# Optimization experiments

Measured on AMD Instinct MI355X. Metric: run time of the kernel, lower is better.

Reference implementation:

```python
import jax, jax.numpy as jnp
import numpy as np
import math

B, W, N = 48, 100, 1000
EMB, H, QKV, LOCAL = 128, 8, 16, 100
L = LOCAL + 1  # depot + local_size neighbors


def pos_enc(length):
    # sinusoidal positional encoding, emb_dim even so no pad needed
    nts = EMB // 2
    inv = jnp.exp(jnp.arange(nts, dtype=jnp.float32) * (-math.log(10000.0) / max(nts - 1, 1)))
    pos = jnp.arange(length, dtype=jnp.float32)
    st = pos[:, None] * inv[None, :]
    return jnp.concatenate([jnp.sin(st), jnp.cos(st)], axis=1)  # [length, EMB]


def setup_inputs() -> dict:
    key = jax.random.key(0)
    ks = jax.random.split(key, 11)
    return {
        "theta": jax.random.uniform(ks[0], (B, W, N), dtype=jnp.float32),
        "dist": jax.random.uniform(ks[1], (B, W, N), dtype=jnp.float32),
        "xy": jax.random.uniform(ks[2], (B, W, N, 2), dtype=jnp.float32),
        "norm_demand": jax.random.uniform(ks[3], (B, W, N), dtype=jnp.float32),
        "ninf_mask": jnp.zeros((B, W, N), jnp.float32),
        "init_w": jax.random.normal(ks[4], (3, EMB), dtype=jnp.float32) * 0.1,
        "init_b": jnp.zeros((EMB,), jnp.float32),
        "cur_token": jax.random.uniform(ks[5], (EMB,), minval=-1.0, maxval=1.0, dtype=jnp.float32),
        "Wq": jax.random.normal(ks[6], (EMB, H * QKV), dtype=jnp.float32) * 0.05,
        "Wk": jax.random.normal(ks[7], (EMB, H * QKV), dtype=jnp.float32) * 0.05,
        "Wv": jax.random.normal(ks[8], (EMB, H * QKV), dtype=jnp.float32) * 0.05,
        "Wc_w": jax.random.normal(ks[9], (H * QKV, EMB), dtype=jnp.float32) * 0.05,
        "Wc_b": jnp.zeros((EMB,), jnp.float32),
    }


def reference(theta, dist, xy, norm_demand, ninf_mask, init_w, init_b, cur_token, Wq, Wk, Wv, Wc_w, Wc_b):
    # depot always masked: dist -= mask => depot distance -> +inf
    mask = ninf_mask.at[:, :, 0].set(-jnp.inf)
    dist_eff = dist - mask  # [B,W,N]

    # k smallest distances among non-depot nodes (topk largest=False)
    neg_vals, idx0 = jax.lax.top_k(-dist_eff[:, :, 1:], LOCAL)
    dvals = -neg_vals
    dvals = jnp.where(jnp.isinf(dvals), 0.0, dvals)
    norm_on = (jnp.max(dvals, axis=-1) != 0.0)[..., None]          # [B,W,1]
    norm_fac = jnp.max(dvals, axis=-1, keepdims=True) + 1e-6       # [B,W,1]

    depot = jnp.zeros((B, W, 1), idx0.dtype)
    idx = jnp.concatenate([depot, idx0 + 1], axis=-1)              # [B,W,L]

    g = lambda a: jnp.take_along_axis(a, idx, axis=-1)
    sd = g(dist_eff)
    sdem = g(norm_demand)
    sm = g(ninf_mask)
    sx = g(xy[..., 0])
    sy = g(xy[..., 1])

    # zero out inf entries (the masked depot slot)
    infm = jnp.isinf(sd)
    sdem = jnp.where(infm, 0.0, sdem)
    sx = jnp.where(infm, 0.0, sx)
    sy = jnp.where(infm, 0.0, sy)

    # per-(b,w) coordinate normalization by max local distance
    sx = jnp.where(norm_on, sx / norm_fac, sx)
    sy = jnp.where(norm_on, sy / norm_fac, sy)

    # euclidean + demand => 3 input features
    sorted_input = jnp.stack([sx, sy, sdem], axis=-1)              # [B,W,L,3]
    init_k = sorted_input @ init_w + init_b + pos_enc(L)[None, None]  # [B,W,L,EMB]

    # cur_token is identical for every (b,w) -> shared query per head
    q = (cur_token @ Wq).reshape(H, QKV)
    k = (init_k @ Wk).reshape(B, W, L, H, QKV)
    v = (init_k @ Wv).reshape(B, W, L, H, QKV)

    score = jnp.einsum('hd,bwlhd->bwhl', q, k) / float(np.sqrt(QKV)) + sm[:, :, None, :]
    attn = jax.nn.softmax(score, axis=-1)
    out = jnp.einsum('bwhl,bwlhd->bwhd', attn, v).reshape(B, W, H * QKV)

    mh = out @ Wc_w + Wc_b                                         # [B,W,EMB]
    score2 = jnp.einsum('bwe,bwle->bwl', mh, init_k) / float(np.sqrt(EMB))

    bi = jnp.arange(B)[:, None, None]
    wi = jnp.arange(W)[None, :, None]
    return jnp.zeros((B, W, N), score2.dtype).at[bi, wi, idx].set(score2)
```

## Files before the change

kernel.cpp:

```cpp
#include <hip/hip_runtime.h>
#include <math.h>

#define Bb   48
#define Ww   100
#define Nn   1000
#define EMB  128
#define Hh   8
#define LL   101
#define LOCALK 100
#define TPB  128
#define PPB  2

typedef _Float16 half2v __attribute__((ext_vector_type(2)));
typedef _Float16 half8v __attribute__((ext_vector_type(8)));

#define WS_A    0
#define WS_PE   1024
#define WS_AC   13952
#define WS_WVI  13984
#define WS_PEA  14496
#define WS_PEH  15304
#define WS_PVH  21768
#define WS_WCT  28424

#define AR_SIZE 7584

#define WSYNC() do { __builtin_amdgcn_wave_barrier(); asm volatile("" ::: "memory"); } while (0)

__device__ __forceinline__ unsigned f2key(float x) {
    unsigned u = __float_as_uint(x);
    return (u & 0x80000000u) ? ~u : (u | 0x80000000u);
}
__device__ __forceinline__ float key2f(unsigned k) {
    unsigned u = (k & 0x80000000u) ? (k & 0x7fffffffu) : ~k;
    return __uint_as_float(u);
}
__device__ __forceinline__ void dot8(float& c0, float& c1, float& c2, float& c3,
                                     half8v p, half8v a) {
    c0 = __builtin_amdgcn_fdot2(__builtin_shufflevector(p, p, 0, 1),
                                __builtin_shufflevector(a, a, 0, 1), c0, false);
    c1 = __builtin_amdgcn_fdot2(__builtin_shufflevector(p, p, 2, 3),
                                __builtin_shufflevector(a, a, 2, 3), c1, false);
    c2 = __builtin_amdgcn_fdot2(__builtin_shufflevector(p, p, 4, 5),
                                __builtin_shufflevector(a, a, 4, 5), c2, false);
    c3 = __builtin_amdgcn_fdot2(__builtin_shufflevector(p, p, 6, 7),
                                __builtin_shufflevector(a, a, 6, 7), c3, false);
}

__global__ void setup1(const float* __restrict__ cur, const float* __restrict__ Wq,
                       const float* __restrict__ Wk, const float* __restrict__ iw,
                       const float* __restrict__ ib, const float* __restrict__ Wv,
                       float* __restrict__ ws) {
    const int t = threadIdx.x, b = blockIdx.x;
    if (b == 0) {
        __shared__ float qs[EMB];
        __shared__ float as_[Hh * EMB];
        if (t < EMB) {
            float acc = 0.f;
            for (int e = 0; e < EMB; ++e) acc += cur[e] * Wq[e * EMB + t];
            qs[t] = acc;
        }
        __syncthreads();
        for (int i = t; i < Hh * EMB; i += 256) {
            int h = i >> 7, e = i & 127;
            float acc = 0.f;
            for (int d = 0; d < 16; ++d) acc += Wk[e * EMB + h * 16 + d] * qs[h * 16 + d];
            acc *= 0.25f;
            as_[i] = acc; ws[WS_A + i] = acc;
        }
        __syncthreads();
        if (t < 32) {
            int i = t >> 3, h = t & 7;
            const float* src = (i == 0) ? iw : (i == 1) ? iw + EMB : (i == 2) ? iw + 2 * EMB : ib;
            float acc = 0.f;
            for (int e = 0; e < EMB; ++e) acc += src[e] * as_[h * EMB + e];
            ws[WS_AC + t] = acc;
        }
    } else {
        int base = (b - 1) * 256 + t;
        const float kneg = -0.14619587891040738f;
        if (base < LL * EMB) {
            int l = base >> 7, c = base & 127, ic = c & 63;
            float inv = expf((float)ic * kneg);
            float v = (float)l * inv;
            float r = (c < 64) ? sinf(v) : cosf(v);
            ws[WS_PE + base] = r;
            ((_Float16*)(ws + WS_PEH))[base] = (_Float16)r;
        } else if (base < LL * EMB + 512) {
            int j = base - LL * EMB;
            int iv = j >> 7, hd = j & 127;
            const float* src = (iv == 0) ? iw : (iv == 1) ? iw + EMB : (iv == 2) ? iw + 2 * EMB : ib;
            float acc = 0.f;
            for (int e = 0; e < EMB; ++e) acc += src[e] * Wv[e * EMB + hd];
            ws[WS_WVI + j] = acc;
        }
    }
}

__global__ void setup2a(const float* __restrict__ Wv, float* __restrict__ ws) {
    int idx = blockIdx.x * 256 + threadIdx.x;
    if (idx < 128 * 104) {
        int hd = idx / 104, l = idx - hd * 104;
        float acc = 0.f;
        if (l < LL) {
            const float* pr = ws + WS_PE + l * EMB;
            for (int e = 0; e < EMB; ++e) acc += pr[e] * Wv[e * EMB + hd];
        }
        ((_Float16*)(ws + WS_PVH))[idx] = (_Float16)acc;
    } else if (idx < 128 * 104 + Hh * LL) {
        int j = idx - 128 * 104;
        int h = j / LL, l = j - h * LL;
        const float* pr = ws + WS_PE + l * EMB;
        const float* ar = ws + WS_A + h * EMB;
        float acc = 0.f;
        for (int e = 0; e < EMB; ++e) acc += pr[e] * ar[e];
        ws[WS_PEA + j] = acc;
    }
}

__global__ void setup2b(const float* __restrict__ Wcw, float* __restrict__ ws) {
    int idx = blockIdx.x * 256 + threadIdx.x;
    if (idx < 128 * 128) {
        int e = idx >> 7, hd = idx & 127;
        ((_Float16*)(ws + WS_WCT))[idx] = (_Float16)Wcw[hd * EMB + e];
    }
}

__global__ __launch_bounds__(TPB, 5) void main_kernel(
    const float* __restrict__ dist,
    const float* __restrict__ xy,
    const float* __restrict__ ndem,
    const float* __restrict__ ninf,
    const float* __restrict__ iw,
    const float* __restrict__ ib,
    const float* __restrict__ Wcb,
    const float* __restrict__ ws,
    float* __restrict__ out) {

    __shared__ __align__(16) char smem[PPB][AR_SIZE];
    const int tid  = threadIdx.x;
    const int w    = tid >> 6;
    const int lane = tid & 63;
    const int bw   = blockIdx.x * PPB + w;

    char* A = smem[w];
    int*                hist4 = (int*)A;
    _Float16*           attnh = (_Float16*)A;
    _Float16*           uhh   = (_Float16*)(A + 1792);
    float*              row   = (float*)A;
    unsigned long long* list  = (unsigned long long*)(A + 4288);
    int*                sel   = (int*)(A + 5088);
    unsigned char*      perm  = (unsigned char*)(A + 5492);
    float*              smk   = (float*)(A + 5592);
    float*              feat3 = (float*)(A + 5996);
    _Float16*           mhh   = (_Float16*)(A + 7216);
    float*              coef  = (float*)(A + 7472);
    float*              coefM = (float*)(A + 7568);

    const float* distRow = dist + (size_t)bw * Nn;
    const float* maskRow = ninf + (size_t)bw * Nn;
    const float* xyRow   = xy   + (size_t)bw * Nn * 2;
    const float* demRow  = ndem + (size_t)bw * Nn;

    float dvf[16], mkf[16];
    {
        float4 dv[4], mv[4];
        #pragma unroll
        for (int c = 0; c < 4; ++c) {
            int n0 = c * 256 + lane * 4;
            if (n0 < Nn) {
                dv[c] = *(const float4*)(distRow + n0);
                mv[c] = *(const float4*)(maskRow + n0);
            } else {
                dv[c] = make_float4(0.f, 0.f, 0.f, 0.f);
                mv[c] = make_float4(0.f, 0.f, 0.f, 0.f);
            }
        }
        #pragma unroll
        for (int k = 0; k < 5; ++k) {
            int idx = lane + 64 * k;
            if (idx < 260) ((int4*)hist4)[idx] = make_int4(0, 0, 0, 0);
        }
        #pragma unroll
        for (int c = 0; c < 4; ++c) {
            dvf[4*c+0] = dv[c].x; dvf[4*c+1] = dv[c].y; dvf[4*c+2] = dv[c].z; dvf[4*c+3] = dv[c].w;
            mkf[4*c+0] = mv[c].x; mkf[4*c+1] = mv[c].y; mkf[4*c+2] = mv[c].z; mkf[4*c+3] = mv[c].w;
        }
    }
    unsigned long long rk[16];
    #pragma unroll
    for (int r = 0; r < 16; ++r) {
        int n = (r >> 2) * 256 + lane * 4 + (r & 3);
        unsigned long long kv = ~0ull;
        if (n >= 1 && n < Nn) {
            float de = dvf[r] - mkf[r];
            kv = ((unsigned long long)f2key(de) << 32) | (unsigned)n;
        }
        rk[r] = kv;
    }
    WSYNC();

    unsigned long long prefix = 0;
    int shift = 56;
    int remRank = 99;
    const unsigned long long ltm = (1ull << lane) - 1ull;
    const int g0 = (lane >> 4) * 260;
    for (int round = 0; round < 8; ++round) {
        shift = 56 - 8 * round;
        #pragma unroll
        for (int r = 0; r < 16; ++r) {
            unsigned long long kv = rk[r];
            bool in = (kv != ~0ull) &&
                      (round == 0 || (kv >> (shift + 8)) == (prefix >> (shift + 8)));
            if (in) atomicAdd(&hist4[g0 + (int)((kv >> shift) & 0xffull)], 1);
        }
        WSYNC();
        int4 h0 = *(int4*)&hist4[0 * 260 + 4 * lane];
        int4 h1 = *(int4*)&hist4[1 * 260 + 4 * lane];
        int4 h2 = *(int4*)&hist4[2 * 260 + 4 * lane];
        int4 h3 = *(int4*)&hist4[3 * 260 + 4 * lane];
        int4 z = make_int4(0, 0, 0, 0);
        *(int4*)&hist4[0 * 260 + 4 * lane] = z;
        *(int4*)&hist4[1 * 260 + 4 * lane] = z;
        *(int4*)&hist4[2 * 260 + 4 * lane] = z;
        *(int4*)&hist4[3 * 260 + 4 * lane] = z;
        int cx = h0.x + h1.x + h2.x + h3.x;
        int cy = h0.y + h1.y + h2.y + h3.y;
        int cz = h0.z + h1.z + h2.z + h3.z;
        int cw = h0.w + h1.w + h2.w + h3.w;
        int s = cx + cy + cz + cw;
        int incl = s;
        #pragma unroll
        for (int o = 1; o < 64; o <<= 1) { int t = __shfl_up(incl, o, 64); if (lane >= o) incl += t; }
        int e0 = incl - s;
        int e1 = e0 + cx, e2 = e1 + cy, e3 = e2 + cz;
        int bc = -1, ec = 0, cc = 0;
        if (cx > 0 && remRank >= e0 && remRank < e1)      { bc = 4*lane+0; ec = e0; cc = cx; }
        if (cy > 0 && remRank >= e1 && remRank < e2)      { bc = 4*lane+1; ec = e1; cc = cy; }
        if (cz > 0 && remRank >= e2 && remRank < e3)      { bc = 4*lane+2; ec = e2; cc = cz; }
        if (cw > 0 && remRank >= e3 && remRank < e3 + cw) { bc = 4*lane+3; ec = e3; cc = cw; }
        unsigned long long fm = __ballot(bc >= 0);
        int srcl = __ffsll((unsigned long long)fm) - 1;
        bc = __shfl(bc, srcl, 64); ec = __shfl(ec, srcl, 64); cc = __shfl(cc, srcl, 64);
        prefix |= ((unsigned long long)(unsigned)bc) << shift;
        remRank -= ec;
        if (cc == 1) break;
    }
    unsigned long long pk = 0; bool pf = false;
    #pragma unroll
    for (int r = 0; r < 16; ++r)
        if ((rk[r] >> shift) == (prefix >> shift)) { pk = rk[r]; pf = true; }
    {
        unsigned long long fm = __ballot(pf);
        int srcl = __ffsll((unsigned long long)fm) - 1;
        pk = __shfl(pk, srcl, 64);
    }
    const unsigned long long pivot = pk;

    int cnt_run = 0;
    #pragma unroll
    for (int r = 0; r < 16; ++r) {
        bool p = rk[r] <= pivot;
        unsigned long long m = __ballot(p);
        if (p) list[cnt_run + (int)__popcll(m & ltm)] = rk[r];
        cnt_run += (int)__popcll(m);
    }
    WSYNC();

    {
        unsigned long long kv0 = list[lane];
        const bool has1 = lane < (LOCALK - 64);
        unsigned long long kv1 = has1 ? list[lane + 64] : ~0ull;
        int r0 = 0, r1 = 0;
        #pragma unroll 4
        for (int j = 0; j < LOCALK; ++j) {
            unsigned long long lv = list[j];
            r0 += (lv < kv0);
            r1 += (lv < kv1);
        }
        float v0 = key2f((unsigned)(kv0 >> 32));
        float dvm = isinf(v0) ? 0.f : v0;
        perm[lane] = (unsigned char)(r0 + 1);
        if (has1) {
            float v1 = key2f((unsigned)(kv1 >> 32));
            perm[lane + 64] = (unsigned char)(r1 + 1);
            dvm = fmaxf(dvm, isinf(v1) ? 0.f : v1);
        }
        #pragma unroll
        for (int o = 32; o > 0; o >>= 1) dvm = fmaxf(dvm, __shfl_xor(dvm, o, 64));
        const float nmax = dvm;
        const bool  norm_on = (nmax != 0.f);
        const float nfac = nmax + 1e-6f;
        WSYNC();

        int crun = 0;
        #pragma unroll
        for (int half = 0; half < 2; ++half) {
            float xs[8], ys[8], dd[8];
            #pragma unroll
            for (int cl = 0; cl < 2; ++cl) {
                int c = half * 2 + cl;
                int n0 = c * 256 + lane * 4;
                float4 a0, a1, d0;
                if (n0 < Nn) {
                    a0 = *(const float4*)(xyRow + 2 * n0);
                    a1 = *(const float4*)(xyRow + 2 * n0 + 4);
                    d0 = *(const float4*)(demRow + n0);
                } else {
                    a0 = a1 = d0 = make_float4(0.f, 0.f, 0.f, 0.f);
                }
                xs[4*cl+0] = a0.x; ys[4*cl+0] = a0.y;
                xs[4*cl+1] = a0.z; ys[4*cl+1] = a0.w;
                xs[4*cl+2] = a1.x; ys[4*cl+2] = a1.y;
                xs[4*cl+3] = a1.z; ys[4*cl+3] = a1.w;
                dd[4*cl+0] = d0.x; dd[4*cl+1] = d0.y; dd[4*cl+2] = d0.z; dd[4*cl+3] = d0.w;
            }
            #pragma unroll
            for (int q = 0; q < 8; ++q) {
                int r = half * 8 + q;
                unsigned long long kv = rk[r];
                bool p = kv <= pivot;
                unsigned long long m = __ballot(p);
                int pos = crun + (int)__popcll(m & ltm);
                crun += (int)__popcll(m);
                if (p) {
                    int rnk = perm[pos];
                    float val = key2f((unsigned)(kv >> 32));
                    bool infm = isinf(val);
                    float fx = infm ? 0.f : xs[q];
                    float fy = infm ? 0.f : ys[q];
                    float fd = infm ? 0.f : dd[q];
                    if (norm_on) { fx /= nfac; fy /= nfac; }
                    int n = (int)(kv & 0xffffffu);
                    feat3[rnk] = fx; feat3[101 + rnk] = fy; feat3[202 + rnk] = fd;
                    smk[rnk] = mkf[r];
                    sel[rnk] = n | (infm ? 0x40000000 : 0);
                }
            }
        }
        if (lane == 0) {
            feat3[0] = 0.f; feat3[101] = 0.f; feat3[202] = 0.f;
            smk[0] = mkf[0];
            sel[0] = 0x40000000;
        }
    }
    WSYNC();

    const int h = lane >> 3, ln8 = lane & 7;
    {
        const float A0 = ws[WS_AC + h], A1 = ws[WS_AC + 8 + h];
        const float A2 = ws[WS_AC + 16 + h], Cc = ws[WS_AC + 24 + h];
        const float* pea = ws + WS_PEA + h * LL;
        float ev[14];
        float mx = -INFINITY;
        #pragma unroll
        for (int k = 0; k < 14; ++k) {
            int l = ln8 + 8 * k;
            float sv = -INFINITY;
            if (l < LL)
                sv = feat3[l] * A0 + feat3[101 + l] * A1 + feat3[202 + l] * A2
                   + Cc + pea[l] + smk[l];
            ev[k] = sv;
            mx = fmaxf(mx, sv);
        }
        #pragma unroll
        for (int o = 1; o < 8; o <<= 1) mx = fmaxf(mx, __shfl_xor(mx, o, 64));
        float sm = 0.f;
        #pragma unroll
        for (int k = 0; k < 14; ++k) {
            int l = ln8 + 8 * k;
            float e = (l < LL) ? __expf(ev[k] - mx) : 0.f;
            ev[k] = e; sm += e;
        }
        #pragma unroll
        for (int o = 1; o < 8; o <<= 1) sm += __shfl_xor(sm, o, 64);
        const float ainv = 1.f / sm;
        #pragma unroll
        for (int k = 0; k < 14; ++k) {
            int l = ln8 + 8 * k;
            attnh[h * 112 + l] = (_Float16)(ev[k] * ainv);
        }
        float c0 = 0.f, c1 = 0.f, c2 = 0.f;
        #pragma unroll
        for (int k = 0; k < 13; ++k) {
            int l = ln8 + 8 * k;
            if (l < LL) {
                float at = ev[k] * ainv;
                c0 += at * feat3[l]; c1 += at * feat3[101 + l]; c2 += at * feat3[202 + l];
            }
        }
        #pragma unroll
        for (int o = 1; o < 8; o <<= 1) {
            c0 += __shfl_xor(c0, o, 64); c1 += __shfl_xor(c1, o, 64); c2 += __shfl_xor(c2, o, 64);
        }
        if (ln8 == 0) { coef[h * 3 + 0] = c0; coef[h * 3 + 1] = c1; coef[h * 3 + 2] = c2; }
    }
    WSYNC();

    #pragma unroll
    for (int t = 0; t < 2; ++t) {
        int hd = lane + 64 * t;
        int hh = hd >> 4;
        const half8v* pv = (const half8v*)((const _Float16*)(ws + WS_PVH) + hd * 104);
        const half8v* at = (const half8v*)(attnh + hh * 112);
        float d0 = 0.f, d1 = 0.f, d2 = 0.f, d3 = 0.f;
        #pragma unroll
        for (int j = 0; j < 13; ++j) dot8(d0, d1, d2, d3, pv[j], at[j]);
        float u = (d0 + d1) + (d2 + d3)
                + coef[hh * 3 + 0] * ws[WS_WVI + hd]
                + coef[hh * 3 + 1] * ws[WS_WVI + 128 + hd]
                + coef[hh * 3 + 2] * ws[WS_WVI + 256 + hd]
                + ws[WS_WVI + 384 + hd];
        uhh[hd] = (_Float16)u;
    }
    WSYNC();

    #pragma unroll
    for (int t = 0; t < 2; ++t) {
        int e = lane + 64 * t;
        const half8v* wr = (const half8v*)((const _Float16*)(ws + WS_WCT) + e * 128);
        const half8v* ur = (const half8v*)uhh;
        float d0 = 0.f, d1 = 0.f, d2 = 0.f, d3 = 0.f;
        #pragma unroll
        for (int j = 0; j < 16; ++j) dot8(d0, d1, d2, d3, wr[j], ur[j]);
        mhh[e] = (_Float16)(Wcb[e] + (d0 + d1) + (d2 + d3));
    }
    WSYNC();

    {
        int g = lane & 3;
        const float* src = (g == 0) ? iw : (g == 1) ? iw + EMB : (g == 2) ? iw + 2 * EMB : ib;
        float v = 0.f;
        #pragma unroll
        for (int j = 0; j < 8; ++j) {
            int e = (lane >> 2) + 16 * j;
            v += (float)mhh[e] * src[e];
        }
        v += __shfl_xor(v, 4, 64); v += __shfl_xor(v, 8, 64);
        v += __shfl_xor(v, 16, 64); v += __shfl_xor(v, 32, 64);
        if (lane < 4) coefM[lane] = v;
    }
    {
        float4 z = make_float4(0.f, 0.f, 0.f, 0.f);
        ((float4*)row)[lane] = z;
        ((float4*)row)[lane + 64] = z;
        ((float4*)row)[lane + 128] = z;
        if (lane < 58) ((float4*)row)[lane + 192] = z;
    }
    WSYNC();

    auto score2 = [&](int t) {
        float base = feat3[t] * coefM[0] + feat3[101 + t] * coefM[1]
                   + feat3[202 + t] * coefM[2] + coefM[3];
        const half8v* pr = (const half8v*)((const _Float16*)(ws + WS_PEH) + t * 128);
        const half8v* mr = (const half8v*)mhh;
        float d0 = 0.f, d1 = 0.f, d2 = 0.f, d3 = 0.f;
        #pragma unroll
        for (int j = 0; j < 16; ++j) dot8(d0, d1, d2, d3, pr[j], mr[j]);
        row[sel[t] & 0xffffff] = (base + (d0 + d1) + (d2 + d3)) * 0.08838834764831845f;
    };
    score2(lane);
    if (lane < LL - 64) score2(lane + 64);
    WSYNC();

    float* outRow = out + (size_t)bw * Nn;
    ((float4*)outRow)[lane]       = ((float4*)row)[lane];
    ((float4*)outRow)[lane + 64]  = ((float4*)row)[lane + 64];
    ((float4*)outRow)[lane + 128] = ((float4*)row)[lane + 128];
    if (lane < 58) ((float4*)outRow)[lane + 192] = ((float4*)row)[lane + 192];
}

extern "C" void kernel_launch(void* const* d_in, const int* in_sizes, int n_in,
                              void* d_out, int out_size, void* d_ws, size_t ws_size,
                              hipStream_t stream) {
    const float* dist  = (const float*)d_in[1];
    const float* xy    = (const float*)d_in[2];
    const float* ndem  = (const float*)d_in[3];
    const float* ninf  = (const float*)d_in[4];
    const float* initw = (const float*)d_in[5];
    const float* initb = (const float*)d_in[6];
    const float* cur   = (const float*)d_in[7];
    const float* Wq    = (const float*)d_in[8];
    const float* Wk    = (const float*)d_in[9];
    const float* Wv    = (const float*)d_in[10];
    const float* Wcw   = (const float*)d_in[11];
    const float* Wcb   = (const float*)d_in[12];
    float* out = (float*)d_out;
    float* ws  = (float*)d_ws;

    hipLaunchKernelGGL(setup1,  dim3(56), dim3(256), 0, stream, cur, Wq, Wk, initw, initb, Wv, ws);
    hipLaunchKernelGGL(setup2a, dim3(56), dim3(256), 0, stream, Wv, ws);
    hipLaunchKernelGGL(setup2b, dim3(64), dim3(256), 0, stream, Wcw, ws);
    hipLaunchKernelGGL(main_kernel, dim3(Bb * Ww / PPB), dim3(TPB), 0, stream,
                       dist, xy, ndem, ninf, initw, initb, Wcb, ws, out);
}
```

Before: 101.6 us.

## Switch attention/projection dot products from fp16 fdot2 to fp32 with transposed layouts

```diff
diff --git a/kernel.cpp b/kernel.cpp
--- a/kernel.cpp
+++ b/kernel.cpp
@@ -11,19 +11,24 @@
 #define TPB  128
 #define PPB  2
 
-typedef _Float16 half2v __attribute__((ext_vector_type(2)));
-typedef _Float16 half8v __attribute__((ext_vector_type(8)));
+typedef float f4v __attribute__((ext_vector_type(4)));
 
 #define WS_A    0
 #define WS_PE   1024
 #define WS_AC   13952
 #define WS_WVI  13984
 #define WS_PEA  14496
-#define WS_PEH  15304
-#define WS_PVH  21768
-#define WS_WCT  28424
-
-#define AR_SIZE 7584
+#define WS_PVT  15304
+#define WS_PET  28232
+
+#define AR_SIZE 7840
+#define AR_SEL  5088
+#define AR_PERM 5492
+#define AR_SMK  5592
+#define AR_F3   5996
+#define AR_MHF  7208
+#define AR_COEF 7720
+#define AR_CM   7816
 
 #define WSYNC() do { __builtin_amdgcn_wave_barrier(); asm volatile("" ::: "memory"); } while (0)
 
@@ -34,17 +39,6 @@
 __device__ __forceinline__ float key2f(unsigned k) {
     unsigned u = (k & 0x80000000u) ? (k & 0x7fffffffu) : ~k;
     return __uint_as_float(u);
-}
-__device__ __forceinline__ void dot8(float& c0, float& c1, float& c2, float& c3,
-                                     half8v p, half8v a) {
-    c0 = __builtin_amdgcn_fdot2(__builtin_shufflevector(p, p, 0, 1),
-                                __builtin_shufflevector(a, a, 0, 1), c0, false);
-    c1 = __builtin_amdgcn_fdot2(__builtin_shufflevector(p, p, 2, 3),
-                                __builtin_shufflevector(a, a, 2, 3), c1, false);
-    c2 = __builtin_amdgcn_fdot2(__builtin_shufflevector(p, p, 4, 5),
-                                __builtin_shufflevector(a, a, 4, 5), c2, false);
-    c3 = __builtin_amdgcn_fdot2(__builtin_shufflevector(p, p, 6, 7),
-                                __builtin_shufflevector(a, a, 6, 7), c3, false);
 }
 
 __global__ void setup1(const float* __restrict__ cur, const float* __restrict__ Wq,
@@ -83,9 +77,7 @@
             int l = base >> 7, c = base & 127, ic = c & 63;
             float inv = expf((float)ic * kneg);
             float v = (float)l * inv;
-            float r = (c < 64) ? sinf(v) : cosf(v);
-            ws[WS_PE + base] = r;
-            ((_Float16*)(ws + WS_PEH))[base] = (_Float16)r;
+            ws[WS_PE + base] = (c < 64) ? sinf(v) : cosf(v);
         } else if (base < LL * EMB + 512) {
             int j = base - LL * EMB;
             int iv = j >> 7, hd = j & 127;
@@ -97,18 +89,20 @@
     }
 }
 
-__global__ void setup2a(const float* __restrict__ Wv, float* __restrict__ ws) {
+__global__ void setup2(const float* __restrict__ Wv, float* __restrict__ ws) {
     int idx = blockIdx.x * 256 + threadIdx.x;
-    if (idx < 128 * 104) {
-        int hd = idx / 104, l = idx - hd * 104;
+    if (idx < LL * EMB) {
+        int l = idx >> 7, hd = idx & 127;
+        const float* pr = ws + WS_PE + l * EMB;
         float acc = 0.f;
-        if (l < LL) {
-            const float* pr = ws + WS_PE + l * EMB;
-            for (int e = 0; e < EMB; ++e) acc += pr[e] * Wv[e * EMB + hd];
-        }
-        ((_Float16*)(ws + WS_PVH))[idx] = (_Float16)acc;
-    } else if (idx < 128 * 104 + Hh * LL) {
-        int j = idx - 128 * 104;
+        for (int e = 0; e < EMB; ++e) acc += pr[e] * Wv[e * EMB + hd];
+        ws[WS_PVT + idx] = acc;
+    } else if (idx < LL * EMB + 128 * 128) {
+        int j = idx - LL * EMB;
+        int e = j >> 7, l = j & 127;
+        ws[WS_PET + j] = (l < LL) ? ws[WS_PE + l * EMB + e] : 0.f;
+    } else if (idx < LL * EMB + 128 * 128 + Hh * LL) {
+        int j = idx - (LL * EMB + 128 * 128);
         int h = j / LL, l = j - h * LL;
         const float* pr = ws + WS_PE + l * EMB;
         const float* ar = ws + WS_A + h * EMB;
@@ -118,44 +112,45 @@
     }
 }
 
-__global__ void setup2b(const float* __restrict__ Wcw, float* __restrict__ ws) {
-    int idx = blockIdx.x * 256 + threadIdx.x;
-    if (idx < 128 * 128) {
-        int e = idx >> 7, hd = idx & 127;
-        ((_Float16*)(ws + WS_WCT))[idx] = (_Float16)Wcw[hd * EMB + e];
-    }
-}
-
-__global__ __launch_bounds__(TPB, 5) void main_kernel(
+__global__ __launch_bounds__(TPB, 4) void main_kernel(
     const float* __restrict__ dist,
     const float* __restrict__ xy,
     const float* __restrict__ ndem,
     const float* __restrict__ ninf,
     const float* __restrict__ iw,
     const float* __restrict__ ib,
+    const float* __restrict__ Wcw,
     const float* __restrict__ Wcb,
     const float* __restrict__ ws,
     float* __restrict__ out) {
 
     __shared__ __align__(16) char smem[PPB][AR_SIZE];
+    __shared__ __align__(16) float sPEA[Hh * LL + 32];
+
     const int tid  = threadIdx.x;
     const int w    = tid >> 6;
     const int lane = tid & 63;
-    const int bw   = blockIdx.x * PPB + w;
+    const int bid  = blockIdx.x;
+    const int bw   = ((bid & 7) * 300 + (bid >> 3)) * PPB + w;
+
+    for (int i = tid; i < Hh * LL + 32; i += TPB)
+        sPEA[i] = (i < Hh * LL) ? ws[WS_PEA + i] : ws[WS_AC + (i - Hh * LL)];
+    __syncthreads();
+    const float* sAC = sPEA + Hh * LL;
 
     char* A = smem[w];
     int*                hist4 = (int*)A;
-    _Float16*           attnh = (_Float16*)A;
-    _Float16*           uhh   = (_Float16*)(A + 1792);
+    float*              attnf = (float*)A;
+    float*              uhf   = (float*)(A + 3232);
     float*              row   = (float*)A;
     unsigned long long* list  = (unsigned long long*)(A + 4288);
-    int*                sel   = (int*)(A + 5088);
-    unsigned char*      perm  = (unsigned char*)(A + 5492);
-    float*              smk   = (float*)(A + 5592);
-    float*              feat3 = (float*)(A + 5996);
-    _Float16*           mhh   = (_Float16*)(A + 7216);
-    float*              coef  = (float*)(A + 7472);
-    float*              coefM = (float*)(A + 7568);
+    int*                sel   = (int*)(A + AR_SEL);
+    unsigned char*      perm  = (unsigned char*)(A + AR_PERM);
+    float*              smk   = (float*)(A + AR_SMK);
+    float*              feat3 = (float*)(A + AR_F3);
+    float*              mhf   = (float*)(A + AR_MHF);
+    float*              coef  = (float*)(A + AR_COEF);
+    float*              coefM = (float*)(A + AR_CM);
 
     const float* distRow = dist + (size_t)bw * Nn;
     const float* maskRow = ninf + (size_t)bw * Nn;
@@ -267,6 +262,27 @@
     }
     WSYNC();
 
+    float xs[16], ys[16], dd[16];
+    {
+        #pragma unroll
+        for (int c = 0; c < 4; ++c) {
+            int n0 = c * 256 + lane * 4;
+            float4 a0, a1, d0;
+            if (n0 < Nn) {
+                a0 = *(const float4*)(xyRow + 2 * n0);
+                a1 = *(const float4*)(xyRow + 2 * n0 + 4);
+                d0 = *(const float4*)(demRow + n0);
+            } else {
+                a0 = a1 = d0 = make_float4(0.f, 0.f, 0.f, 0.f);
+            }
+            xs[4*c+0] = a0.x; ys[4*c+0] = a0.y;
+            xs[4*c+1] = a0.z; ys[4*c+1] = a0.w;
+            xs[4*c+2] = a1.x; ys[4*c+2] = a1.y;
+            xs[4*c+3] = a1.z; ys[4*c+3] = a1.w;
+            dd[4*c+0] = d0.x; dd[4*c+1] = d0.y; dd[4*c+2] = d0.z; dd[4*c+3] = d0.w;
+        }
+    }
+
     {
         unsigned long long kv0 = list[lane];
         const bool has1 = lane < (LOCALK - 64);
@@ -295,47 +311,24 @@
 
         int crun = 0;
         #pragma unroll
-        for (int half = 0; half < 2; ++half) {
-            float xs[8], ys[8], dd[8];
-            #pragma unroll
-            for (int cl = 0; cl < 2; ++cl) {
-                int c = half * 2 + cl;
-                int n0 = c * 256 + lane * 4;
-                float4 a0, a1, d0;
-                if (n0 < Nn) {
-                    a0 = *(const float4*)(xyRow + 2 * n0);
-                    a1 = *(const float4*)(xyRow + 2 * n0 + 4);
-                    d0 = *(const float4*)(demRow + n0);
-                } else {
-                    a0 = a1 = d0 = make_float4(0.f, 0.f, 0.f, 0.f);
-                }
-                xs[4*cl+0] = a0.x; ys[4*cl+0] = a0.y;
-                xs[4*cl+1] = a0.z; ys[4*cl+1] = a0.w;
-                xs[4*cl+2] = a1.x; ys[4*cl+2] = a1.y;
-                xs[4*cl+3] = a1.z; ys[4*cl+3] = a1.w;
-                dd[4*cl+0] = d0.x; dd[4*cl+1] = d0.y; dd[4*cl+2] = d0.z; dd[4*cl+3] = d0.w;
-            }
-            #pragma unroll
-            for (int q = 0; q < 8; ++q) {
-                int r = half * 8 + q;
-                unsigned long long kv = rk[r];
-                bool p = kv <= pivot;
-                unsigned long long m = __ballot(p);
-                int pos = crun + (int)__popcll(m & ltm);
-                crun += (int)__popcll(m);
-                if (p) {
-                    int rnk = perm[pos];
-                    float val = key2f((unsigned)(kv >> 32));
-                    bool infm = isinf(val);
-                    float fx = infm ? 0.f : xs[q];
-                    float fy = infm ? 0.f : ys[q];
-                    float fd = infm ? 0.f : dd[q];
-                    if (norm_on) { fx /= nfac; fy /= nfac; }
-                    int n = (int)(kv & 0xffffffu);
-                    feat3[rnk] = fx; feat3[101 + rnk] = fy; feat3[202 + rnk] = fd;
-                    smk[rnk] = mkf[r];
-                    sel[rnk] = n | (infm ? 0x40000000 : 0);
-                }
+        for (int r = 0; r < 16; ++r) {
+            unsigned long long kv = rk[r];
+            bool p = kv <= pivot;
+            unsigned long long m = __ballot(p);
+            int pos = crun + (int)__popcll(m & ltm);
+            crun += (int)__popcll(m);
+            if (p) {
+                int rnk = perm[pos];
+                float val = key2f((unsigned)(kv >> 32));
+                bool infm = isinf(val);
+                float fx = infm ? 0.f : xs[r];
+                float fy = infm ? 0.f : ys[r];
+                float fd = infm ? 0.f : dd[r];
+                if (norm_on) { fx /= nfac; fy /= nfac; }
+                int n = (int)(kv & 0xffffffu);
+                feat3[rnk] = fx; feat3[101 + rnk] = fy; feat3[202 + rnk] = fd;
+                smk[rnk] = mkf[r];
+                sel[rnk] = n | (infm ? 0x40000000 : 0);
             }
         }
         if (lane == 0) {
@@ -348,9 +341,8 @@
 
     const int h = lane >> 3, ln8 = lane & 7;
     {
-        const float A0 = ws[WS_AC + h], A1 = ws[WS_AC + 8 + h];
-        const float A2 = ws[WS_AC + 16 + h], Cc = ws[WS_AC + 24 + h];
-        const float* pea = ws + WS_PEA + h * LL;
+        const float A0 = sAC[h], A1 = sAC[8 + h], A2 = sAC[16 + h], Cc = sAC[24 + h];
+        const float* pea = sPEA + h * LL;
         float ev[14];
         float mx = -INFINITY;
         #pragma unroll
@@ -375,17 +367,13 @@
         #pragma unroll
         for (int o = 1; o < 8; o <<= 1) sm += __shfl_xor(sm, o, 64);
         const float ainv = 1.f / sm;
+        float c0 = 0.f, c1 = 0.f, c2 = 0.f;
         #pragma unroll
         for (int k = 0; k < 14; ++k) {
-            int l = ln8 + 8 * k;
-            attnh[h * 112 + l] = (_Float16)(ev[k] * ainv);
-        }
-        float c0 = 0.f, c1 = 0.f, c2 = 0.f;
-        #pragma unroll
-        for (int k = 0; k < 13; ++k) {
             int l = ln8 + 8 * k;
             if (l < LL) {
                 float at = ev[k] * ainv;
+                attnf[h * LL + l] = at;
                 c0 += at * feat3[l]; c1 += at * feat3[101 + l]; c2 += at * feat3[202 + l];
             }
         }
@@ -397,33 +385,38 @@
     }
     WSYNC();
 
-    #pragma unroll
-    for (int t = 0; t < 2; ++t) {
-        int hd = lane + 64 * t;
-        int hh = hd >> 4;
-        const half8v* pv = (const half8v*)((const _Float16*)(ws + WS_PVH) + hd * 104);
-        const half8v* at = (const half8v*)(attnh + hh * 112);
-        float d0 = 0.f, d1 = 0.f, d2 = 0.f, d3 = 0.f;
-        #pragma unroll
-        for (int j = 0; j < 13; ++j) dot8(d0, d1, d2, d3, pv[j], at[j]);
-        float u = (d0 + d1) + (d2 + d3)
-                + coef[hh * 3 + 0] * ws[WS_WVI + hd]
-                + coef[hh * 3 + 1] * ws[WS_WVI + 128 + hd]
-                + coef[hh * 3 + 2] * ws[WS_WVI + 256 + hd]
-                + ws[WS_WVI + 384 + hd];
-        uhh[hd] = (_Float16)u;
-    }
-    WSYNC();
-
-    #pragma unroll
-    for (int t = 0; t < 2; ++t) {
-        int e = lane + 64 * t;
-        const half8v* wr = (const half8v*)((const _Float16*)(ws + WS_WCT) + e * 128);
-        const half8v* ur = (const half8v*)uhh;
-        float d0 = 0.f, d1 = 0.f, d2 = 0.f, d3 = 0.f;
-        #pragma unroll
-        for (int j = 0; j < 16; ++j) dot8(d0, d1, d2, d3, wr[j], ur[j]);
-        mhh[e] = (_Float16)(Wcb[e] + (d0 + d1) + (d2 + d3));
+    {
+        float u0 = 0.f, u1 = 0.f;
+        const float* arow = attnf + h * LL;
+        const float2* pvt = (const float2*)(ws + WS_PVT) + lane;
+        #pragma unroll 4
+        for (int l = 0; l < LL; ++l) {
+            float a = arow[l];
+            float2 p = pvt[(size_t)l * 64];
+            u0 += a * p.x; u1 += a * p.y;
+        }
+        float2 w0 = *(const float2*)(ws + WS_WVI + 2 * lane);
+        float2 w1 = *(const float2*)(ws + WS_WVI + 128 + 2 * lane);
+        float2 w2 = *(const float2*)(ws + WS_WVI + 256 + 2 * lane);
+        float2 w3 = *(const float2*)(ws + WS_WVI + 384 + 2 * lane);
+        float cc0 = coef[h * 3 + 0], cc1 = coef[h * 3 + 1], cc2 = coef[h * 3 + 2];
+        u0 += cc0 * w0.x + cc1 * w1.x + cc2 * w2.x + w3.x;
+        u1 += cc0 * w0.y + cc1 * w1.y + cc2 * w2.y + w3.y;
+        *(float2*)(uhf + 2 * lane) = make_float2(u0, u1);
+    }
+    WSYNC();
+
+    {
+        float2 wb = *(const float2*)(Wcb + 2 * lane);
+        float m0 = wb.x, m1 = wb.y;
+        const float2* wc = (const float2*)Wcw + lane;
+        #pragma unroll 4
+        for (int hd = 0; hd < EMB; ++hd) {
+            float uu = uhf[hd];
+            float2 wv = wc[(size_t)hd * 64];
+            m0 += uu * wv.x; m1 += uu * wv.y;
+        }
+        *(float2*)(mhf + 2 * lane) = make_float2(m0, m1);
     }
     WSYNC();
 
@@ -434,7 +427,7 @@
         #pragma unroll
         for (int j = 0; j < 8; ++j) {
             int e = (lane >> 2) + 16 * j;
-            v += (float)mhh[e] * src[e];
+            v += mhf[e] * src[e];
         }
         v += __shfl_xor(v, 4, 64); v += __shfl_xor(v, 8, 64);
         v += __shfl_xor(v, 16, 64); v += __shfl_xor(v, 32, 64);
@@ -449,25 +442,41 @@
     }
     WSYNC();
 
-    auto score2 = [&](int t) {
-        float base = feat3[t] * coefM[0] + feat3[101 + t] * coefM[1]
-                   + feat3[202 + t] * coefM[2] + coefM[3];
-        const half8v* pr = (const half8v*)((const _Float16*)(ws + WS_PEH) + t * 128);
-        const half8v* mr = (const half8v*)mhh;
-        float d0 = 0.f, d1 = 0.f, d2 = 0.f, d3 = 0.f;
-        #pragma unroll
-        for (int j = 0; j < 16; ++j) dot8(d0, d1, d2, d3, pr[j], mr[j]);
-        row[sel[t] & 0xffffff] = (base + (d0 + d1) + (d2 + d3)) * 0.08838834764831845f;
-    };
-    score2(lane);
-    if (lane < LL - 64) score2(lane + 64);
+    {
+        float s0 = 0.f, s1 = 0.f;
+        const float* pet = ws + WS_PET;
+        #pragma unroll 4
+        for (int e = 0; e < EMB; ++e) {
+            float mv = mhf[e];
+            const float* pr = pet + (size_t)e * 128;
+            s0 += mv * pr[lane];
+            s1 += mv * pr[lane + 64];
+        }
+        const float scale = 0.08838834764831845f;
+        {
+            int t = lane;
+            float base = feat3[t] * coefM[0] + feat3[101 + t] * coefM[1]
+                       + feat3[202 + t] * coefM[2] + coefM[3];
+            row[sel[t] & 0xffffff] = (base + s0) * scale;
+        }
+        if (lane + 64 < LL) {
+            int t = lane + 64;
+            float base = feat3[t] * coefM[0] + feat3[101 + t] * coefM[1]
+                       + feat3[202 + t] * coefM[2] + coefM[3];
+            row[sel[t] & 0xffffff] = (base + s1) * scale;
+        }
+    }
     WSYNC();
 
     float* outRow = out + (size_t)bw * Nn;
-    ((float4*)outRow)[lane]       = ((float4*)row)[lane];
-    ((float4*)outRow)[lane + 64]  = ((float4*)row)[lane + 64];
-    ((float4*)outRow)[lane + 128] = ((float4*)row)[lane + 128];
-    if (lane < 58) ((float4*)outRow)[lane + 192] = ((float4*)row)[lane + 192];
+    #pragma unroll
+    for (int c = 0; c < 4; ++c) {
+        int i = lane + 64 * c;
+        if (i < 250) {
+            f4v v = *(const f4v*)(row + 4 * i);
+            __builtin_nontemporal_store(v, (f4v*)(outRow + 4 * i));
+        }
+    }
 }
 
 extern "C" void kernel_launch(void* const* d_in, const int* in_sizes, int n_in,
@@ -488,9 +497,8 @@
     float* out = (float*)d_out;
     float* ws  = (float*)d_ws;
 
-    hipLaunchKernelGGL(setup1,  dim3(56), dim3(256), 0, stream, cur, Wq, Wk, initw, initb, Wv, ws);
-    hipLaunchKernelGGL(setup2a, dim3(56), dim3(256), 0, stream, Wv, ws);
-    hipLaunchKernelGGL(setup2b, dim3(64), dim3(256), 0, stream, Wcw, ws);
+    hipLaunchKernelGGL(setup1, dim3(56),  dim3(256), 0, stream, cur, Wq, Wk, initw, initb, Wv, ws);
+    hipLaunchKernelGGL(setup2, dim3(118), dim3(256), 0, stream, Wv, ws);
     hipLaunchKernelGGL(main_kernel, dim3(Bb * Ww / PPB), dim3(TPB), 0, stream,
-                       dist, xy, ndem, ninf, initw, initb, Wcb, ws, out);
+                       dist, xy, ndem, ninf, initw, initb, Wcw, Wcb, ws, out);
 }
```

Measured after the change: 115.5 us. 13.7% more time.
